# Performance work log

Hardware: AMD Instinct MI355X
Metric: run time of the kernel (lower is better)

## Reference

```python
import jax, jax.numpy as jnp
import numpy as np

B, S, I, H, O, L = 64, 512, 256, 512, 256, 2


def setup_inputs() -> dict:
    key = jax.random.key(0)
    ks = jax.random.split(key, 8)
    s = 0.02
    return {
        "x": jax.random.normal(ks[0], (B, S, I), dtype=jnp.float32),
        "input_W": jax.random.normal(ks[1], (H, I), dtype=jnp.float32) * s,
        "input_b": jnp.zeros((H,), dtype=jnp.float32),
        "i2h_W": jax.random.normal(ks[2], (L, H, H), dtype=jnp.float32) * s,
        "h2h_W": jax.random.normal(ks[3], (L, H, H), dtype=jnp.float32) * s,
        "h2h_b": jnp.zeros((L, H), dtype=jnp.float32),
        "out_W": jax.random.normal(ks[4], (O, H), dtype=jnp.float32) * s,
        "out_b": jnp.zeros((O,), dtype=jnp.float32),
    }


def reference(x, input_W, input_b, i2h_W, h2h_W, h2h_b, out_W, out_b):
    # input projection applied to the whole sequence at once, as in the source
    xe = jnp.einsum("bsi,hi->bsh", x, input_W) + input_b  # [B,S,H]

    def step(h, x_t):  # h: [L,B,H], x_t: [B,H]
        cur = x_t
        new_h = []
        for l in range(L):
            cur = jnp.tanh(cur @ i2h_W[l].T + h[l] @ h2h_W[l].T + h2h_b[l])
            new_h.append(cur)
        return jnp.stack(new_h), None

    h0 = jnp.zeros((L, B, H), dtype=x.dtype)
    hT, _ = jax.lax.scan(step, h0, jnp.swapaxes(xe, 0, 1))  # scan over S
    output = hT[-1] @ out_W.T + out_b  # [B,O]
    return output, hT
```

## Files before the change

### kernel.cpp

```cpp
#include <hip/hip_runtime.h>

typedef __attribute__((ext_vector_type(8))) short bf16x8;
typedef __attribute__((ext_vector_type(4))) float f32x4;

#define NWG 128

__device__ __forceinline__ unsigned short f2bf(float f) {
  union { float f; unsigned u; } v; v.f = f;
  unsigned r = v.u + 0x7FFFu + ((v.u >> 16) & 1u);
  return (unsigned short)(r >> 16);
}

__device__ __forceinline__ float bf2f(unsigned short u) {
  union { unsigned u; float f; } v; v.u = (unsigned)u << 16;
  return v.f;
}

__device__ __forceinline__ float fast_tanh(float x) {
  float ax = fminf(fabsf(x), 15.f);
  float e = __expf(2.f * ax);
  float t = (e - 1.f) / (e + 1.f);
  return copysignf(t, x);
}

#define LDH(d, b, O) \
  asm volatile("global_load_dwordx4 %0, %1, off offset:" #O " sc0 sc1" : "=v"(d) : "v"(b))
#define LDH16(A, B)            \
  LDH(A[0], B, 0);   LDH(A[1], B, 64);  LDH(A[2], B, 128); LDH(A[3], B, 192);  \
  LDH(A[4], B, 256); LDH(A[5], B, 320); LDH(A[6], B, 384); LDH(A[7], B, 448);  \
  LDH(A[8], B, 512); LDH(A[9], B, 576); LDH(A[10], B, 640); LDH(A[11], B, 704); \
  LDH(A[12], B, 768); LDH(A[13], B, 832); LDH(A[14], B, 896); LDH(A[15], B, 960)

__device__ __forceinline__ void wait_flags(const unsigned* p, unsigned tgt) {
  while (true) {
    unsigned v;
    asm volatile("global_load_dword %0, %1, off sc0 sc1\n\t"
                 "s_waitcnt vmcnt(0)"
                 : "=v"(v) : "v"(p) : "memory");
    if (__all((int)(v >= tgt))) break;
  }
}

__global__ void prep_kernel(const float* __restrict__ i2h,
                            const float* __restrict__ h2h,
                            unsigned short* __restrict__ WiB,
                            unsigned short* __restrict__ WhB,
                            unsigned short* __restrict__ h0,
                            unsigned short* __restrict__ h1,
                            unsigned* __restrict__ bar,
                            unsigned* __restrict__ flags) {
  int i = blockIdx.x * 256 + threadIdx.x;
  WiB[i] = f2bf(i2h[i]);
  WhB[i] = f2bf(h2h[i]);
  if (i < 65536) { h0[i] = 0; h1[i] = 0; }
  if (i < 64) bar[i] = 0;
  if (i < 4096) flags[i] = 0;
}

__global__ __launch_bounds__(256) void wc_kernel(const float* __restrict__ inW,
                                                 const float* __restrict__ inb,
                                                 const float* __restrict__ i2h,
                                                 const float* __restrict__ hb,
                                                 unsigned short* __restrict__ WcB,
                                                 float* __restrict__ bc) {
  const int n = blockIdx.x, i = threadIdx.x;
  const float* wrow = i2h + (size_t)n * 512;
  float acc = 0.f;
  for (int k = 0; k < 512; ++k) acc += wrow[k] * inW[k * 256 + i];
  WcB[n * 256 + i] = f2bf(acc);
  if (i == 0) {
    float a2 = 0.f;
    for (int k = 0; k < 512; ++k) a2 += wrow[k] * inb[k];
    bc[n] = a2 + hb[n];
  }
}

__global__ __launch_bounds__(256) void proj_kernel(const float* __restrict__ x,
                                                   const unsigned short* __restrict__ WcB,
                                                   const float* __restrict__ bc,
                                                   unsigned short* __restrict__ U) {
  const int tid = threadIdx.x;
  const int ln = tid & 63, wv = tid >> 6;
  const int wid = blockIdx.x * 4 + wv;
  const int mt = wid >> 5, nt = wid & 31;
  const int mrow = ln & 15, quad = ln >> 4, koff = quad * 8;
  const float* arow = x + (size_t)(mt * 16 + mrow) * 256 + koff;
  const unsigned short* brow = WcB + (size_t)(nt * 16 + mrow) * 256 + koff;
  f32x4 acc = {0.f, 0.f, 0.f, 0.f};
#pragma unroll
  for (int kk = 0; kk < 8; ++kk) {
    const int ko = kk * 32;
    bf16x8 af;
#pragma unroll
    for (int j = 0; j < 8; ++j) af[j] = (short)f2bf(arow[ko + j]);
    bf16x8 bf = *(const bf16x8*)(brow + ko);
    acc = __builtin_amdgcn_mfma_f32_16x16x32_bf16(af, bf, acc, 0, 0, 0);
  }
  const int n = nt * 16 + mrow;
  const float bias = bc[n];
  const int m0 = mt * 16 + quad * 4;
#pragma unroll
  for (int r = 0; r < 4; ++r) {
    const int m = m0 + r;
    const int b = m >> 9, s = m & 511;
    U[((size_t)(s * 64 + b) << 9) + n] = f2bf(acc[r] + bias);
  }
}

__device__ __forceinline__ void heavy_barrier(unsigned* bar) {
  __builtin_amdgcn_s_waitcnt(0);
  __syncthreads();
  if (threadIdx.x == 0) {
    __threadfence();
    unsigned prev = __hip_atomic_fetch_add(bar, 1u, __ATOMIC_RELAXED, __HIP_MEMORY_SCOPE_AGENT);
    if (prev == NWG - 1) {
      __hip_atomic_store(bar + 32, 1u, __ATOMIC_RELAXED, __HIP_MEMORY_SCOPE_AGENT);
    } else {
      while (__hip_atomic_load(bar + 32, __ATOMIC_RELAXED, __HIP_MEMORY_SCOPE_AGENT) < 1u)
        __builtin_amdgcn_s_sleep(1);
    }
    __threadfence();
  }
  __syncthreads();
}

__device__ __forceinline__ void store_h_coh(unsigned* dbase, int rowbase, int colp,
                                            bool evenl,
                                            float v0, float v1, float v2, float v3) {
  unsigned lo = (unsigned)f2bf(v0) | ((unsigned)f2bf(v1) << 16);
  unsigned hi = (unsigned)f2bf(v2) | ((unsigned)f2bf(v3) << 16);
  unsigned send = evenl ? hi : lo;
  unsigned recv = __shfl_xor(send, 1, 64);
  unsigned w0, w1; int rb;
  if (evenl) {
    w0 = (lo & 0xffffu) | (recv << 16);
    w1 = (lo >> 16) | (recv & 0xffff0000u);
    rb = rowbase;
  } else {
    w0 = (recv & 0xffffu) | (hi << 16);
    w1 = (recv >> 16) | (hi & 0xffff0000u);
    rb = rowbase + 2;
  }
  unsigned* p = dbase + rb * 256 + colp;
  __hip_atomic_store(p, w0, __ATOMIC_RELAXED, __HIP_MEMORY_SCOPE_AGENT);
  __hip_atomic_store(p + 256, w1, __ATOMIC_RELAXED, __HIP_MEMORY_SCOPE_AGENT);
}

__global__ __launch_bounds__(64, 1) void scan_kernel(const unsigned short* __restrict__ U,
                                                     const unsigned short* __restrict__ WiB,
                                                     const unsigned short* __restrict__ WhB,
                                                     const float* __restrict__ hb,
                                                     const float* __restrict__ outW,
                                                     const float* __restrict__ outb,
                                                     unsigned short* __restrict__ h0,
                                                     unsigned short* __restrict__ h1,
                                                     float* __restrict__ out,
                                                     unsigned* __restrict__ bar,
                                                     unsigned* __restrict__ flags) {
  const int ln = threadIdx.x;
  const int wid = blockIdx.x;
  const int rt = wid & 3;
  const int ct = wid >> 2;
  const int mrow = ln & 15, quad = ln >> 4, koff = quad * 8;
  const int bA = rt * 16 + mrow;
  const int n = ct * 16 + mrow;
  const bool evenl = (ln & 1) == 0;
  const int colp = n >> 1;
  const int rowbase = rt * 16 + quad * 4;

  bf16x8 wf0[16], wf1[16], wf2[16];
  {
    const unsigned short* w0 = WhB + (size_t)n * 512 + koff;
    const unsigned short* w1 = WiB + (size_t)262144 + (size_t)n * 512 + koff;
    const unsigned short* w2 = WhB + (size_t)262144 + (size_t)n * 512 + koff;
#pragma unroll
    for (int kk = 0; kk < 16; ++kk) {
      wf0[kk] = *(const bf16x8*)(w0 + kk * 32);
      wf1[kk] = *(const bf16x8*)(w1 + kk * 32);
      wf2[kk] = *(const bf16x8*)(w2 + kk * 32);
    }
  }
  const float bias1 = hb[512 + n];
  const unsigned short* h0b = h0 + (size_t)bA * 512 + koff;
  const unsigned short* h1b = h1 + (size_t)bA * 512 + koff;
  const unsigned short* UB = U + ((size_t)rowbase << 9) + n;
  unsigned* myflag = flags + ((rt * 32 + ct) << 5);
  const unsigned* pollp = flags + ((rt * 32 + (ln & 31)) << 5);

  unsigned short up0 = UB[0], up1 = UB[512], up2 = UB[1024], up3 = UB[1536];

  for (int s = 0; s <= 512; ++s) {
    const int pd = s & 1, ps = pd ^ 1;
    if (s) wait_flags(pollp, (unsigned)s);

    const unsigned short* aH0 = h0b + (ps << 15);
    const unsigned short* aH1 = h1b + (pd << 15);
    bf16x8 h0f[16], h1f[16];
    LDH16(h0f, aH0);
    LDH16(h1f, aH1);
    asm volatile("s_waitcnt vmcnt(0)" ::: "memory");
#pragma unroll
    for (int kk = 0; kk < 16; ++kk) {
      asm volatile("" : "+v"(h0f[kk]));
      asm volatile("" : "+v"(h1f[kk]));
    }

    f32x4 z = {0.f, 0.f, 0.f, 0.f};
    f32x4 acc0 = z, a1a = z, a1b = z;
    const bool D0 = (s < 512), D1 = (s > 0);
#pragma unroll
    for (int kk = 0; kk < 16; ++kk) {
      if (D0) acc0 = __builtin_amdgcn_mfma_f32_16x16x32_bf16(h0f[kk], wf0[kk], acc0, 0, 0, 0);
      if (D1) {
        a1a = __builtin_amdgcn_mfma_f32_16x16x32_bf16(h0f[kk], wf1[kk], a1a, 0, 0, 0);
        a1b = __builtin_amdgcn_mfma_f32_16x16x32_bf16(h1f[kk], wf2[kk], a1b, 0, 0, 0);
      }
    }

    if (D0) {
      float v0 = fast_tanh(acc0[0] + bf2f(up0));
      float v1 = fast_tanh(acc0[1] + bf2f(up1));
      float v2 = fast_tanh(acc0[2] + bf2f(up2));
      float v3 = fast_tanh(acc0[3] + bf2f(up3));
      store_h_coh((unsigned*)h0 + (pd << 14), rowbase, colp, evenl, v0, v1, v2, v3);
      if (s == 511) {
        float* o = out + 16384 + rowbase * 512 + n;
        o[0] = v0; o[512] = v1; o[1024] = v2; o[1536] = v3;
      }
    }
    if (D1) {
      float v0 = fast_tanh(a1a[0] + a1b[0] + bias1);
      float v1 = fast_tanh(a1a[1] + a1b[1] + bias1);
      float v2 = fast_tanh(a1a[2] + a1b[2] + bias1);
      float v3 = fast_tanh(a1a[3] + a1b[3] + bias1);
      store_h_coh((unsigned*)h1 + (ps << 14), rowbase, colp, evenl, v0, v1, v2, v3);
      if (s == 512) {
        float* o = out + 16384 + 32768 + rowbase * 512 + n;
        o[0] = v0; o[512] = v1; o[1024] = v2; o[1536] = v3;
      }
    }

    asm volatile("s_waitcnt vmcnt(0)" ::: "memory");
    if (ln == 0) {
      unsigned fv = (unsigned)(s + 1);
      asm volatile("global_store_dword %0, %1, off sc0 sc1" :: "v"(myflag), "v"(fv) : "memory");
    }

    if (s <= 510) {
      const unsigned short* un = UB + ((size_t)(s + 1) << 15);
      up0 = un[0]; up1 = un[512]; up2 = un[1024]; up3 = un[1536];
    }
  }

  heavy_barrier(bar);

  const int g = blockIdx.x * 64 + ln;
  const float* hT1 = out + 16384 + 32768;
#pragma unroll
  for (int e = 0; e < 2; ++e) {
    const int idx = g + e * 8192;
    const int b = idx >> 8, o = idx & 255;
    const float* hr = hT1 + (b << 9);
    const float* wr = outW + (o << 9);
    float s0 = 0.f, s1 = 0.f;
    for (int k = 0; k < 512; k += 8) {
      float4 h4 = *(const float4*)(hr + k);
      float4 w4 = *(const float4*)(wr + k);
      s0 += h4.x * w4.x + h4.y * w4.y + h4.z * w4.z + h4.w * w4.w;
      float4 h5 = *(const float4*)(hr + k + 4);
      float4 w5 = *(const float4*)(wr + k + 4);
      s1 += h5.x * w5.x + h5.y * w5.y + h5.z * w5.z + h5.w * w5.w;
    }
    out[idx] = s0 + s1 + outb[o];
  }
}

extern "C" void kernel_launch(void* const* d_in, const int* in_sizes, int n_in,
                              void* d_out, int out_size, void* d_ws, size_t ws_size,
                              hipStream_t stream) {
  const float* x = (const float*)d_in[0];
  const float* inW = (const float*)d_in[1];
  const float* inb = (const float*)d_in[2];
  const float* i2h = (const float*)d_in[3];
  const float* h2h = (const float*)d_in[4];
  const float* hbias = (const float*)d_in[5];
  const float* outW = (const float*)d_in[6];
  const float* outb = (const float*)d_in[7];
  float* out = (float*)d_out;

  char* w = (char*)d_ws;
  unsigned short* WiB = (unsigned short*)w;
  unsigned short* WhB = (unsigned short*)(w + (1u << 20));
  unsigned short* WcB = (unsigned short*)(w + (2u << 20));
  float* bc = (float*)(w + (2u << 20) + (256u << 10));
  unsigned short* h0 = (unsigned short*)(w + (2u << 20) + (260u << 10));
  unsigned short* h1 = (unsigned short*)(w + (2u << 20) + (388u << 10));
  unsigned* bar = (unsigned*)(w + (2u << 20) + (516u << 10));
  unsigned* flags = (unsigned*)(w + (2u << 20) + (520u << 10));
  unsigned short* U = (unsigned short*)(w + (2u << 20) + (576u << 10));

  prep_kernel<<<2048, 256, 0, stream>>>(i2h, h2h, WiB, WhB, h0, h1, bar, flags);
  wc_kernel<<<512, 256, 0, stream>>>(inW, inb, i2h, hbias, WcB, bc);
  proj_kernel<<<16384, 256, 0, stream>>>(x, WcB, bc, U);
  scan_kernel<<<NWG, 64, 0, stream>>>(U, WiB, WhB, hbias, outW, outb, h0, h1, out, bar, flags);
}
```

Baseline: 2.100 ms.

## Replace per-step flag polling with tag bits embedded in hidden-state data

The separate flag array and its poll loop are removed. Instead, the low mantissa bit of each stored bf16 pair carries a step-parity tag, and readers spin on the hidden-state loads themselves until every tag matches. The next step's hidden-state and U loads are issued speculatively right after the layer-0 store, overlapping them with layer-1 work. Dropping the flag write/read round trip is meant to cut per-step synchronization latency. The cost is a corrupted LSB in bf16 values, weaker cache-coherence bits on loads and stores, and a bounded-guard spin that could silently proceed with stale data.

```diff
diff --git a/kernel.cpp b/kernel.cpp
--- a/kernel.cpp
+++ b/kernel.cpp
@@ -2,6 +2,7 @@
 
 typedef __attribute__((ext_vector_type(8))) short bf16x8;
 typedef __attribute__((ext_vector_type(4))) float f32x4;
+typedef __attribute__((ext_vector_type(4))) unsigned u32x4;
 
 #define NWG 128
 
@@ -11,8 +12,8 @@
   return (unsigned short)(r >> 16);
 }
 
-__device__ __forceinline__ float bf2f(unsigned short u) {
-  union { unsigned u; float f; } v; v.u = (unsigned)u << 16;
+__device__ __forceinline__ float bf2f(unsigned u) {
+  union { unsigned u; float f; } v; v.u = u << 16;
   return v.f;
 }
 
@@ -24,22 +25,14 @@
 }
 
 #define LDH(d, b, O) \
-  asm volatile("global_load_dwordx4 %0, %1, off offset:" #O " sc0 sc1" : "=v"(d) : "v"(b))
+  asm volatile("global_load_dwordx4 %0, %1, off offset:" #O " sc1" : "=v"(d) : "v"(b))
 #define LDH16(A, B)            \
   LDH(A[0], B, 0);   LDH(A[1], B, 64);  LDH(A[2], B, 128); LDH(A[3], B, 192);  \
   LDH(A[4], B, 256); LDH(A[5], B, 320); LDH(A[6], B, 384); LDH(A[7], B, 448);  \
   LDH(A[8], B, 512); LDH(A[9], B, 576); LDH(A[10], B, 640); LDH(A[11], B, 704); \
   LDH(A[12], B, 768); LDH(A[13], B, 832); LDH(A[14], B, 896); LDH(A[15], B, 960)
-
-__device__ __forceinline__ void wait_flags(const unsigned* p, unsigned tgt) {
-  while (true) {
-    unsigned v;
-    asm volatile("global_load_dword %0, %1, off sc0 sc1\n\t"
-                 "s_waitcnt vmcnt(0)"
-                 : "=v"(v) : "v"(p) : "memory");
-    if (__all((int)(v >= tgt))) break;
-  }
-}
+#define LDU(d, p) \
+  asm volatile("global_load_ushort %0, %1, off" : "=v"(d) : "v"(p))
 
 __global__ void prep_kernel(const float* __restrict__ i2h,
                             const float* __restrict__ h2h,
@@ -47,14 +40,12 @@
                             unsigned short* __restrict__ WhB,
                             unsigned short* __restrict__ h0,
                             unsigned short* __restrict__ h1,
-                            unsigned* __restrict__ bar,
-                            unsigned* __restrict__ flags) {
+                            unsigned* __restrict__ bar) {
   int i = blockIdx.x * 256 + threadIdx.x;
   WiB[i] = f2bf(i2h[i]);
   WhB[i] = f2bf(h2h[i]);
-  if (i < 65536) { h0[i] = 0; h1[i] = 0; }
+  if (i < 65536) { h0[i] = (i >= 32768) ? 0x0001 : 0; h1[i] = 0; }
   if (i < 64) bar[i] = 0;
-  if (i < 4096) flags[i] = 0;
 }
 
 __global__ __launch_bounds__(256) void wc_kernel(const float* __restrict__ inW,
@@ -124,8 +115,8 @@
   __syncthreads();
 }
 
-__device__ __forceinline__ void store_h_coh(unsigned* dbase, int rowbase, int colp,
-                                            bool evenl,
+__device__ __forceinline__ void store_h_tag(unsigned* dbase, int rowbase, int colp,
+                                            bool evenl, unsigned tagpat,
                                             float v0, float v1, float v2, float v3) {
   unsigned lo = (unsigned)f2bf(v0) | ((unsigned)f2bf(v1) << 16);
   unsigned hi = (unsigned)f2bf(v2) | ((unsigned)f2bf(v3) << 16);
@@ -141,9 +132,11 @@
     w1 = (recv >> 16) | (hi & 0xffff0000u);
     rb = rowbase + 2;
   }
+  w0 = (w0 & ~1u) | tagpat;
+  w1 = (w1 & ~1u) | tagpat;
   unsigned* p = dbase + rb * 256 + colp;
-  __hip_atomic_store(p, w0, __ATOMIC_RELAXED, __HIP_MEMORY_SCOPE_AGENT);
-  __hip_atomic_store(p + 256, w1, __ATOMIC_RELAXED, __HIP_MEMORY_SCOPE_AGENT);
+  asm volatile("global_store_dword %0, %1, off sc1" :: "v"(p), "v"(w0) : "memory");
+  asm volatile("global_store_dword %0, %1, off offset:1024 sc1" :: "v"(p), "v"(w1) : "memory");
 }
 
 __global__ __launch_bounds__(64, 1) void scan_kernel(const unsigned short* __restrict__ U,
@@ -155,8 +148,7 @@
                                                      unsigned short* __restrict__ h0,
                                                      unsigned short* __restrict__ h1,
                                                      float* __restrict__ out,
-                                                     unsigned* __restrict__ bar,
-                                                     unsigned* __restrict__ flags) {
+                                                     unsigned* __restrict__ bar) {
   const int ln = threadIdx.x;
   const int wid = blockIdx.x;
   const int rt = wid & 3;
@@ -184,30 +176,65 @@
   const unsigned short* h0b = h0 + (size_t)bA * 512 + koff;
   const unsigned short* h1b = h1 + (size_t)bA * 512 + koff;
   const unsigned short* UB = U + ((size_t)rowbase << 9) + n;
-  unsigned* myflag = flags + ((rt * 32 + ct) << 5);
-  const unsigned* pollp = flags + ((rt * 32 + (ln & 31)) << 5);
-
-  unsigned short up0 = UB[0], up1 = UB[512], up2 = UB[1024], up3 = UB[1536];
+
+  bf16x8 h0f[16], h1f[16];
+  unsigned up0, up1, up2, up3;
+  {
+    const unsigned short* aH0 = h0b + (1 << 15);
+    const unsigned short* aH1 = h1b;
+    LDH16(h0f, aH0);
+    LDH16(h1f, aH1);
+    LDU(up0, UB); LDU(up1, UB + 512); LDU(up2, UB + 1024); LDU(up3, UB + 1536);
+  }
 
   for (int s = 0; s <= 512; ++s) {
     const int pd = s & 1, ps = pd ^ 1;
-    if (s) wait_flags(pollp, (unsigned)s);
-
-    const unsigned short* aH0 = h0b + (ps << 15);
-    const unsigned short* aH1 = h1b + (pd << 15);
-    bf16x8 h0f[16], h1f[16];
-    LDH16(h0f, aH0);
-    LDH16(h1f, aH1);
-    asm volatile("s_waitcnt vmcnt(0)" ::: "memory");
+    const bool D0 = (s < 512), D1 = (s > 0);
+    const unsigned e = s ? (((unsigned)(s - 1) >> 1) & 1u) : 1u;
+
+    if (s == 0 || s == 512) asm volatile("s_waitcnt vmcnt(0)" ::: "memory");
+    else                    asm volatile("s_waitcnt vmcnt(2)" ::: "memory");
 #pragma unroll
     for (int kk = 0; kk < 16; ++kk) {
       asm volatile("" : "+v"(h0f[kk]));
       asm volatile("" : "+v"(h1f[kk]));
     }
+    asm volatile("" : "+v"(up0), "+v"(up1), "+v"(up2), "+v"(up3));
+
+    {
+      int guard = 0;
+      while (true) {
+        unsigned acc = e ? 0xFFFFFFFFu : 0u;
+#pragma unroll
+        for (int kk = 0; kk < 16; ++kk) {
+          u32x4 a = __builtin_bit_cast(u32x4, h0f[kk]);
+          if (e) acc &= a[0] & a[1] & a[2] & a[3];
+          else   acc |= a[0] | a[1] | a[2] | a[3];
+        }
+        if (D1) {
+#pragma unroll
+          for (int kk = 0; kk < 16; ++kk) {
+            u32x4 a = __builtin_bit_cast(u32x4, h1f[kk]);
+            if (e) acc &= a[0] & a[1] & a[2] & a[3];
+            else   acc |= a[0] | a[1] | a[2] | a[3];
+          }
+        }
+        if (__all((int)((acc & 1u) == e)) || ++guard > 4096) break;
+        const unsigned short* aH0 = h0b + (ps << 15);
+        const unsigned short* aH1 = h1b + (pd << 15);
+        LDH16(h0f, aH0);
+        LDH16(h1f, aH1);
+        asm volatile("s_waitcnt vmcnt(0)" ::: "memory");
+#pragma unroll
+        for (int kk = 0; kk < 16; ++kk) {
+          asm volatile("" : "+v"(h0f[kk]));
+          asm volatile("" : "+v"(h1f[kk]));
+        }
+      }
+    }
 
     f32x4 z = {0.f, 0.f, 0.f, 0.f};
     f32x4 acc0 = z, a1a = z, a1b = z;
-    const bool D0 = (s < 512), D1 = (s > 0);
 #pragma unroll
     for (int kk = 0; kk < 16; ++kk) {
       if (D0) acc0 = __builtin_amdgcn_mfma_f32_16x16x32_bf16(h0f[kk], wf0[kk], acc0, 0, 0, 0);
@@ -217,39 +244,42 @@
       }
     }
 
+    const unsigned tagpat = (unsigned)((s >> 1) & 1);
+
     if (D0) {
       float v0 = fast_tanh(acc0[0] + bf2f(up0));
       float v1 = fast_tanh(acc0[1] + bf2f(up1));
       float v2 = fast_tanh(acc0[2] + bf2f(up2));
       float v3 = fast_tanh(acc0[3] + bf2f(up3));
-      store_h_coh((unsigned*)h0 + (pd << 14), rowbase, colp, evenl, v0, v1, v2, v3);
+      store_h_tag((unsigned*)h0 + (pd << 14), rowbase, colp, evenl, tagpat, v0, v1, v2, v3);
       if (s == 511) {
         float* o = out + 16384 + rowbase * 512 + n;
         o[0] = v0; o[512] = v1; o[1024] = v2; o[1536] = v3;
       }
     }
+
+    if (s < 512) {
+      const unsigned short* aH0n = h0b + (pd << 15);
+      const unsigned short* aH1n = h1b + (ps << 15);
+      LDH16(h0f, aH0n);
+      LDH16(h1f, aH1n);
+      if (s < 511) {
+        const unsigned short* un = UB + ((size_t)(s + 1) << 15);
+        LDU(up0, un); LDU(up1, un + 512); LDU(up2, un + 1024); LDU(up3, un + 1536);
+      }
+    }
+
     if (D1) {
       float v0 = fast_tanh(a1a[0] + a1b[0] + bias1);
       float v1 = fast_tanh(a1a[1] + a1b[1] + bias1);
       float v2 = fast_tanh(a1a[2] + a1b[2] + bias1);
       float v3 = fast_tanh(a1a[3] + a1b[3] + bias1);
-      store_h_coh((unsigned*)h1 + (ps << 14), rowbase, colp, evenl, v0, v1, v2, v3);
+      store_h_tag((unsigned*)h1 + (ps << 14), rowbase, colp, evenl, tagpat, v0, v1, v2, v3);
       if (s == 512) {
         float* o = out + 16384 + 32768 + rowbase * 512 + n;
         o[0] = v0; o[512] = v1; o[1024] = v2; o[1536] = v3;
       }
     }
-
-    asm volatile("s_waitcnt vmcnt(0)" ::: "memory");
-    if (ln == 0) {
-      unsigned fv = (unsigned)(s + 1);
-      asm volatile("global_store_dword %0, %1, off sc0 sc1" :: "v"(myflag), "v"(fv) : "memory");
-    }
-
-    if (s <= 510) {
-      const unsigned short* un = UB + ((size_t)(s + 1) << 15);
-      up0 = un[0]; up1 = un[512]; up2 = un[1024]; up3 = un[1536];
-    }
   }
 
   heavy_barrier(bar);
@@ -257,8 +287,8 @@
   const int g = blockIdx.x * 64 + ln;
   const float* hT1 = out + 16384 + 32768;
 #pragma unroll
-  for (int e = 0; e < 2; ++e) {
-    const int idx = g + e * 8192;
+  for (int e2 = 0; e2 < 2; ++e2) {
+    const int idx = g + e2 * 8192;
     const int b = idx >> 8, o = idx & 255;
     const float* hr = hT1 + (b << 9);
     const float* wr = outW + (o << 9);
@@ -296,11 +326,10 @@
   unsigned short* h0 = (unsigned short*)(w + (2u << 20) + (260u << 10));
   unsigned short* h1 = (unsigned short*)(w + (2u << 20) + (388u << 10));
   unsigned* bar = (unsigned*)(w + (2u << 20) + (516u << 10));
-  unsigned* flags = (unsigned*)(w + (2u << 20) + (520u << 10));
   unsigned short* U = (unsigned short*)(w + (2u << 20) + (576u << 10));
 
-  prep_kernel<<<2048, 256, 0, stream>>>(i2h, h2h, WiB, WhB, h0, h1, bar, flags);
+  prep_kernel<<<2048, 256, 0, stream>>>(i2h, h2h, WiB, WhB, h0, h1, bar);
   wc_kernel<<<512, 256, 0, stream>>>(inW, inb, i2h, hbias, WcB, bc);
   proj_kernel<<<16384, 256, 0, stream>>>(x, WcB, bc, U);
-  scan_kernel<<<NWG, 64, 0, stream>>>(U, WiB, WhB, hbias, outW, outb, h0, h1, out, bar, flags);
-}
+  scan_kernel<<<NWG, 64, 0, stream>>>(U, WiB, WhB, hbias, outW, outb, h0, h1, out, bar);
+}
```

After: 3.888 ms. 85.1% more time.
